# Performance work log

Hardware: AMD Instinct MI355X
Metric: run time of the kernel (lower is better)

Reference implementation:

```python
import jax, jax.numpy as jnp
import numpy as np

MARGIN = 0.5


def setup_inputs() -> dict:
    key = jax.random.key(0)
    k1, k2, k3, k4 = jax.random.split(key, 4)
    Ns, Nt, D = 8192, 8192, 512
    return {
        "source_emb": jax.random.normal(k1, (Ns, D), dtype=jnp.float32),
        "target_emb": jax.random.normal(k2, (Nt, D), dtype=jnp.float32),
        "source_sec": jax.random.randint(k3, (Ns,), 0, 6),
        "target_sec": jax.random.randint(k4, (Nt,), 0, 6),
    }


def reference(source_emb, target_emb, source_sec, target_sec):
    D = source_emb.shape[-1]
    Nt = target_emb.shape[0]
    sq_s = jnp.sum(source_emb * source_emb, axis=-1)  # [Ns]
    sq_t = jnp.sum(target_emb * target_emb, axis=-1)  # [Nt]
    gram = jnp.einsum("sd,td->st", source_emb, target_emb)  # [Ns, Nt]
    d2 = jnp.maximum(sq_s[:, None] + sq_t[None, :] - 2.0 * gram, 0.0) / D
    d = jnp.sqrt(d2)
    same = source_sec[:, None] == target_sec[None, :]  # [Ns, Nt] bool
    # semantic: sum of d^2 over matching pairs, divided by Nt
    loss_s = jnp.sum(jnp.where(same, d2, 0.0), axis=1) / Nt
    # contrastive: sum of max(0, margin - d)^2 over non-matching pairs, / Nt
    hinge = jnp.maximum(0.0, MARGIN - d) ** 2
    loss_c = jnp.sum(jnp.where(same, 0.0, hinge), axis=1) / Nt
    return (loss_s, loss_c)
```

## Files before the change

### kernel.cpp

```cpp
#include <hip/hip_runtime.h>
#include <stdint.h>
#include <stddef.h>

#define NS 8192
#define NT 8192
#define DD 512
#define QS 32.0f
#define INV_S2 (1.0f / (QS * QS))
#define INV_DNT (1.0f / ((float)DD * (float)NT))
#define INV_NT  (1.0f / (float)NT)

typedef __attribute__((ext_vector_type(4))) int i32x4;
typedef __attribute__((ext_vector_type(16))) int i32x16;

#define WS_A    ((size_t)0)
#define WS_B    (WS_A + (size_t)NS * DD)
#define WS_SQS  (WS_B + (size_t)NT * DD)
#define WS_SQT  (WS_SQS + (size_t)NS * 4)

__device__ __forceinline__ void gload16(const void* g, void* l) {
  __builtin_amdgcn_global_load_lds(
      (const __attribute__((address_space(1))) unsigned int*)g,
      (__attribute__((address_space(3))) unsigned int*)l, 16, 0, 0);
}

__global__ __launch_bounds__(256) void prep_kernel(
    const float* __restrict__ src, const float* __restrict__ tgt,
    char* __restrict__ ws) {
  const int tid = threadIdx.x, wid = tid >> 6, lane = tid & 63;
  char* Ai8 = ws + WS_A;
  char* Bi8 = ws + WS_B;
  float* sqs = (float*)(ws + WS_SQS);
  float* sqt = (float*)(ws + WS_SQT);

#pragma unroll
  for (int it = 0; it < 4; ++it) {
    const int row = blockIdx.x * 4 + wid + it * 4096;
    const bool isT = row >= NS;
    const int r = isT ? row - NS : row;
    const float* in = (isT ? tgt : src) + (size_t)r * DD;
    const float4* rp = (const float4*)in;
    float4 v0 = rp[lane * 2], v1 = rp[lane * 2 + 1];
    float x[8] = {v0.x, v0.y, v0.z, v0.w, v1.x, v1.y, v1.z, v1.w};
    float ss = 0.f;
    int q[8];
#pragma unroll
    for (int j = 0; j < 8; ++j) {
      ss += x[j] * x[j];
      int qi = __float2int_rn(x[j] * QS);
      q[j] = min(127, max(-127, qi));
    }
    const int lo = (q[0] & 255) | ((q[1] & 255) << 8) |
                   ((q[2] & 255) << 16) | ((q[3] & 255) << 24);
    const int hi = (q[4] & 255) | ((q[5] & 255) << 8) |
                   ((q[6] & 255) << 16) | ((q[7] & 255) << 24);
    *(int2*)((isT ? Bi8 : Ai8) + (size_t)r * DD + lane * 8) = make_int2(lo, hi);
#pragma unroll
    for (int off = 32; off >= 1; off >>= 1) ss += __shfl_xor(ss, off, 64);
    if (lane == 0) (isT ? sqt : sqs)[r] = ss;
  }
}

__global__ __launch_bounds__(256, 2) void gram_kernel(
    const char* __restrict__ ws, const int* __restrict__ ssec,
    const int* __restrict__ tsec, float* __restrict__ out) {
  __shared__ __align__(16) char As[8192];
  __shared__ __align__(16) char Bs[8192];
  __shared__ float ls_red[2][128];
  __shared__ float sq_l[128];
  __shared__ int sec_l[128];

  const float* sqs = (const float*)(ws + WS_SQS);
  const float* sqt = (const float*)(ws + WS_SQT);

  const int lin = blockIdx.x;
  const int xcd = lin & 7, ii = lin >> 3;
  const int m_blk = xcd * 8 + (ii & 7);
  const int n_blk = ii >> 3;
  const int rowA = m_blk * 128, rowB = n_blk * 128;

  const int tid = threadIdx.x, wid = tid >> 6, lane = tid & 63;
  const int wr = wid >> 1, wc = wid & 1;
  const int lh = lane >> 5;

  const char* aSrc[2];
  const char* bSrc[2];
  int ldsDst[2];
#pragma unroll
  for (int ih = 0; ih < 2; ++ih) {
    const int o = ih * 4096 + tid * 16;
    const int row_p = o >> 6;
    const int bl = (o & 63) ^ (((row_p >> 1) & 3) << 4);
    ldsDst[ih] = ih * 4096 + wid * 1024;
    aSrc[ih] = ws + WS_A + (size_t)(rowA + row_p) * DD + bl;
    bSrc[ih] = ws + WS_B + (size_t)(rowB + row_p) * DD + bl;
  }

  int aOff[2][2], bOff[2][2];
#pragma unroll
  for (int mi = 0; mi < 2; ++mi)
#pragma unroll
    for (int kk = 0; kk < 2; ++kk) {
      const int l = kk * 32 + lh * 16;
      const int ra = wr * 64 + mi * 32 + (lane & 31);
      aOff[mi][kk] = ra * 64 + (l ^ (((ra >> 1) & 3) << 4));
      const int rb = wc * 64 + mi * 32 + (lane & 31);
      bOff[mi][kk] = rb * 64 + (l ^ (((rb >> 1) & 3) << 4));
    }

  i32x16 acc[2][2];
#pragma unroll
  for (int mi = 0; mi < 2; ++mi)
#pragma unroll
    for (int ni = 0; ni < 2; ++ni)
#pragma unroll
      for (int j = 0; j < 16; ++j) acc[mi][ni][j] = 0;

  for (int t = 0; t < 8; ++t) {
    const size_t k0 = (size_t)t * 64;
    gload16(aSrc[0] + k0, &As[ldsDst[0]]);
    gload16(aSrc[1] + k0, &As[ldsDst[1]]);
    gload16(bSrc[0] + k0, &Bs[ldsDst[0]]);
    gload16(bSrc[1] + k0, &Bs[ldsDst[1]]);
    __syncthreads();

    i32x4 a[2][2], b[2][2];
#pragma unroll
    for (int mi = 0; mi < 2; ++mi)
#pragma unroll
      for (int kk = 0; kk < 2; ++kk) {
        a[mi][kk] = *(const i32x4*)&As[aOff[mi][kk]];
        b[mi][kk] = *(const i32x4*)&Bs[bOff[mi][kk]];
      }
#pragma unroll
    for (int kk = 0; kk < 2; ++kk)
#pragma unroll
      for (int mi = 0; mi < 2; ++mi)
#pragma unroll
        for (int ni = 0; ni < 2; ++ni)
          acc[mi][ni] = __builtin_amdgcn_mfma_i32_32x32x32_i8(
              a[mi][kk], b[ni][kk], acc[mi][ni], 0, 0, 0);
    __syncthreads();
  }

  if (tid < 128) {
    sq_l[tid] = sqs[rowA + tid];
    sec_l[tid] = ssec[rowA + tid];
  }
  __syncthreads();

  float sqc[2];
  int tc[2];
#pragma unroll
  for (int ni = 0; ni < 2; ++ni) {
    const int gcol = rowB + wc * 64 + ni * 32 + (lane & 31);
    sqc[ni] = sqt[gcol];
    tc[ni] = tsec[gcol];
  }

#pragma unroll
  for (int mi = 0; mi < 2; ++mi) {
#pragma unroll
    for (int reg = 0; reg < 16; ++reg) {
      const int rowin = (reg & 3) + 8 * (reg >> 2) + 4 * lh;
      const int lrow = wr * 64 + mi * 32 + rowin;
      const float sqr = sq_l[lrow];
      const int sc = sec_l[lrow];
      float v = 0.f;
#pragma unroll
      for (int ni = 0; ni < 2; ++ni) {
        const float g = (float)acc[mi][ni][reg] * INV_S2;
        const float d2r = sqr + sqc[ni] - 2.f * g;
        if (sc == tc[ni]) {
          v += fmaxf(d2r, 0.f);
        } else if (d2r < 128.f) {
          const float d = sqrtf(fmaxf(d2r, 0.f) * (1.f / (float)DD));
          const float hh = 0.5f - d;
          atomicAdd(&out[NS + rowA + lrow], hh * hh * INV_NT);
        }
      }
      v += __shfl_xor(v, 1, 64);
      v += __shfl_xor(v, 2, 64);
      v += __shfl_xor(v, 4, 64);
      v += __shfl_xor(v, 8, 64);
      v += __shfl_xor(v, 16, 64);
      if ((lane & 31) == rowin) ls_red[wc][lrow] = v;
    }
  }
  __syncthreads();

  if (tid < 128)
    atomicAdd(&out[rowA + tid], (ls_red[0][tid] + ls_red[1][tid]) * INV_DNT);
}

extern "C" void kernel_launch(void* const* d_in, const int* in_sizes, int n_in,
                              void* d_out, int out_size, void* d_ws, size_t ws_size,
                              hipStream_t stream) {
  const float* src = (const float*)d_in[0];
  const float* tgt = (const float*)d_in[1];
  const int* ssec = (const int*)d_in[2];
  const int* tsec = (const int*)d_in[3];
  float* out = (float*)d_out;
  char* ws = (char*)d_ws;

  hipMemsetAsync(out, 0, (size_t)2 * NS * sizeof(float), stream);
  prep_kernel<<<1024, 256, 0, stream>>>(src, tgt, ws);
  gram_kernel<<<4096, 256, 0, stream>>>(ws, ssec, tsec, out);
}
```

Baseline: 94.62 us.

## Compute semantic loss via per-section target sums and skip epilogue tiles by bound

The semantic loss is computed algebraically from per-section target sums, counts and squared-norm sums, using a new reduction kernel and a per-row dot-product kernel, rather than in the gram epilogue. The gram kernel gains a three-stage LDS prefetch pipeline with explicit waitcnt and barriers. Its epilogue uses a wave-level bound check that skips tiles whose distances all exceed the margin, keeping only a negative-clamp correction for matching pairs. This removes most of the per-element epilogue work and shuffle reductions, at the cost of two extra launches, more atomics and more LDS per block.

```diff
diff --git a/kernel.cpp b/kernel.cpp
--- a/kernel.cpp
+++ b/kernel.cpp
@@ -5,6 +5,7 @@
 #define NS 8192
 #define NT 8192
 #define DD 512
+#define NSEC 6
 #define QS 32.0f
 #define INV_S2 (1.0f / (QS * QS))
 #define INV_DNT (1.0f / ((float)DD * (float)NT))
@@ -17,6 +18,10 @@
 #define WS_B    (WS_A + (size_t)NS * DD)
 #define WS_SQS  (WS_B + (size_t)NT * DD)
 #define WS_SQT  (WS_SQS + (size_t)NS * 4)
+#define WS_TS   (WS_SQT + (size_t)NT * 4)
+#define WS_CNT  (WS_TS + (size_t)NSEC * DD * 4)
+#define WS_SSQ  (WS_CNT + NSEC * 4)
+#define WS_ZEND (WS_SSQ + NSEC * 4)
 
 __device__ __forceinline__ void gload16(const void* g, void* l) {
   __builtin_amdgcn_global_load_lds(
@@ -61,14 +66,83 @@
   }
 }
 
-__global__ __launch_bounds__(256, 2) void gram_kernel(
+__global__ __launch_bounds__(512) void tsum_kernel(
+    const float* __restrict__ tgt, const int* __restrict__ tsec,
+    char* __restrict__ ws) {
+  const int d = threadIdx.x;
+  const int r0 = blockIdx.x * 128;
+  float a[NSEC] = {0.f, 0.f, 0.f, 0.f, 0.f, 0.f};
+  for (int r = 0; r < 128; ++r) {
+    const int sec = tsec[r0 + r];
+    const float v = tgt[(size_t)(r0 + r) * DD + d];
+#pragma unroll
+    for (int c = 0; c < NSEC; ++c) a[c] += (sec == c) ? v : 0.f;
+  }
+  float* ts = (float*)(ws + WS_TS);
+#pragma unroll
+  for (int c = 0; c < NSEC; ++c) atomicAdd(&ts[c * DD + d], a[c]);
+
+  if (threadIdx.x < 64) {
+    const float* sqt = (const float*)(ws + WS_SQT);
+    float cn[NSEC] = {0, 0, 0, 0, 0, 0}, sq[NSEC] = {0, 0, 0, 0, 0, 0};
+#pragma unroll
+    for (int i = 0; i < 2; ++i) {
+      const int r = r0 + i * 64 + threadIdx.x;
+      const int sec = tsec[r];
+      const float qv = sqt[r];
+#pragma unroll
+      for (int c = 0; c < NSEC; ++c) {
+        cn[c] += (sec == c) ? 1.f : 0.f;
+        sq[c] += (sec == c) ? qv : 0.f;
+      }
+    }
+#pragma unroll
+    for (int c = 0; c < NSEC; ++c) {
+#pragma unroll
+      for (int off = 32; off >= 1; off >>= 1) {
+        cn[c] += __shfl_xor(cn[c], off, 64);
+        sq[c] += __shfl_xor(sq[c], off, 64);
+      }
+    }
+    if (threadIdx.x == 0) {
+      float* cnt = (float*)(ws + WS_CNT);
+      float* ssq = (float*)(ws + WS_SSQ);
+#pragma unroll
+      for (int c = 0; c < NSEC; ++c) {
+        atomicAdd(&cnt[c], cn[c]);
+        atomicAdd(&ssq[c], sq[c]);
+      }
+    }
+  }
+}
+
+__global__ __launch_bounds__(256) void ls_kernel(
+    const float* __restrict__ src, const int* __restrict__ ssec,
+    const char* __restrict__ ws, float* __restrict__ out) {
+  const int tid = threadIdx.x, wid = tid >> 6, lane = tid & 63;
+  const int row = blockIdx.x * 4 + wid;
+  const float* tsum = (const float*)(ws + WS_TS);
+  const float* cnt  = (const float*)(ws + WS_CNT);
+  const float* ssq  = (const float*)(ws + WS_SSQ);
+  const float* sqs  = (const float*)(ws + WS_SQS);
+
+  const int c = ssec[row];
+  const float4* rp = (const float4*)(src + (size_t)row * DD);
+  const float4* tp = (const float4*)(tsum + c * DD);
+  float4 a0 = rp[lane * 2], a1 = rp[lane * 2 + 1];
+  float4 b0 = tp[lane * 2], b1 = tp[lane * 2 + 1];
+  float dot = a0.x * b0.x + a0.y * b0.y + a0.z * b0.z + a0.w * b0.w +
+              a1.x * b1.x + a1.y * b1.y + a1.z * b1.z + a1.w * b1.w;
+#pragma unroll
+  for (int off = 32; off >= 1; off >>= 1) dot += __shfl_xor(dot, off, 64);
+  if (lane == 0)
+    out[row] = (cnt[c] * sqs[row] + ssq[c] - 2.f * dot) * INV_DNT;
+}
+
+__global__ __launch_bounds__(256, 3) void gram_kernel(
     const char* __restrict__ ws, const int* __restrict__ ssec,
     const int* __restrict__ tsec, float* __restrict__ out) {
-  __shared__ __align__(16) char As[8192];
-  __shared__ __align__(16) char Bs[8192];
-  __shared__ float ls_red[2][128];
-  __shared__ float sq_l[128];
-  __shared__ int sec_l[128];
+  __shared__ __align__(16) char lds[3][16384];
 
   const float* sqs = (const float*)(ws + WS_SQS);
   const float* sqt = (const float*)(ws + WS_SQT);
@@ -96,6 +170,14 @@
     bSrc[ih] = ws + WS_B + (size_t)(rowB + row_p) * DD + bl;
   }
 
+#define STAGE(T, BUF)                                                   \
+  {                                                                     \
+    gload16(aSrc[0] + (size_t)(T) * 64, &lds[BUF][ldsDst[0]]);          \
+    gload16(aSrc[1] + (size_t)(T) * 64, &lds[BUF][ldsDst[1]]);          \
+    gload16(bSrc[0] + (size_t)(T) * 64, &lds[BUF][8192 + ldsDst[0]]);   \
+    gload16(bSrc[1] + (size_t)(T) * 64, &lds[BUF][8192 + ldsDst[1]]);   \
+  }
+
   int aOff[2][2], bOff[2][2];
 #pragma unroll
   for (int mi = 0; mi < 2; ++mi)
@@ -105,7 +187,7 @@
       const int ra = wr * 64 + mi * 32 + (lane & 31);
       aOff[mi][kk] = ra * 64 + (l ^ (((ra >> 1) & 3) << 4));
       const int rb = wc * 64 + mi * 32 + (lane & 31);
-      bOff[mi][kk] = rb * 64 + (l ^ (((rb >> 1) & 3) << 4));
+      bOff[mi][kk] = 8192 + rb * 64 + (l ^ (((rb >> 1) & 3) << 4));
     }
 
   i32x16 acc[2][2];
@@ -116,21 +198,24 @@
 #pragma unroll
       for (int j = 0; j < 16; ++j) acc[mi][ni][j] = 0;
 
+  STAGE(0, 0)
+  STAGE(1, 1)
+  asm volatile("s_waitcnt vmcnt(4)" ::: "memory");
+  __builtin_amdgcn_sched_barrier(0);
+  __builtin_amdgcn_s_barrier();
+
+#pragma unroll
   for (int t = 0; t < 8; ++t) {
-    const size_t k0 = (size_t)t * 64;
-    gload16(aSrc[0] + k0, &As[ldsDst[0]]);
-    gload16(aSrc[1] + k0, &As[ldsDst[1]]);
-    gload16(bSrc[0] + k0, &Bs[ldsDst[0]]);
-    gload16(bSrc[1] + k0, &Bs[ldsDst[1]]);
-    __syncthreads();
+    const int cur = t % 3;
+    if (t + 2 < 8) STAGE(t + 2, (t + 2) % 3)
 
     i32x4 a[2][2], b[2][2];
 #pragma unroll
     for (int mi = 0; mi < 2; ++mi)
 #pragma unroll
       for (int kk = 0; kk < 2; ++kk) {
-        a[mi][kk] = *(const i32x4*)&As[aOff[mi][kk]];
-        b[mi][kk] = *(const i32x4*)&Bs[bOff[mi][kk]];
+        a[mi][kk] = *(const i32x4*)&lds[cur][aOff[mi][kk]];
+        b[mi][kk] = *(const i32x4*)&lds[cur][bOff[mi][kk]];
       }
 #pragma unroll
     for (int kk = 0; kk < 2; ++kk)
@@ -140,57 +225,70 @@
         for (int ni = 0; ni < 2; ++ni)
           acc[mi][ni] = __builtin_amdgcn_mfma_i32_32x32x32_i8(
               a[mi][kk], b[ni][kk], acc[mi][ni], 0, 0, 0);
-    __syncthreads();
-  }
-
-  if (tid < 128) {
-    sq_l[tid] = sqs[rowA + tid];
-    sec_l[tid] = ssec[rowA + tid];
-  }
-  __syncthreads();
-
+
+    __builtin_amdgcn_sched_barrier(0);
+    if (t + 2 < 8) {
+      asm volatile("s_waitcnt vmcnt(4)" ::: "memory");
+    } else if (t == 6) {
+      asm volatile("s_waitcnt vmcnt(0)" ::: "memory");
+    }
+    __builtin_amdgcn_sched_barrier(0);
+    if (t < 7) __builtin_amdgcn_s_barrier();
+  }
+#undef STAGE
+
+  const int colc = lane & 31;
   float sqc[2];
-  int tc[2];
-#pragma unroll
-  for (int ni = 0; ni < 2; ++ni) {
-    const int gcol = rowB + wc * 64 + ni * 32 + (lane & 31);
-    sqc[ni] = sqt[gcol];
-    tc[ni] = tsec[gcol];
-  }
-
-#pragma unroll
-  for (int mi = 0; mi < 2; ++mi) {
-#pragma unroll
-    for (int reg = 0; reg < 16; ++reg) {
-      const int rowin = (reg & 3) + 8 * (reg >> 2) + 4 * lh;
-      const int lrow = wr * 64 + mi * 32 + rowin;
-      const float sqr = sq_l[lrow];
-      const int sc = sec_l[lrow];
-      float v = 0.f;
-#pragma unroll
-      for (int ni = 0; ni < 2; ++ni) {
-        const float g = (float)acc[mi][ni][reg] * INV_S2;
-        const float d2r = sqr + sqc[ni] - 2.f * g;
-        if (sc == tc[ni]) {
-          v += fmaxf(d2r, 0.f);
-        } else if (d2r < 128.f) {
-          const float d = sqrtf(fmaxf(d2r, 0.f) * (1.f / (float)DD));
-          const float hh = 0.5f - d;
-          atomicAdd(&out[NS + rowA + lrow], hh * hh * INV_NT);
+#pragma unroll
+  for (int ni = 0; ni < 2; ++ni)
+    sqc[ni] = sqt[rowB + wc * 64 + ni * 32 + colc];
+
+  float smin = sqs[rowA + wr * 64 + lane];
+#pragma unroll
+  for (int off = 32; off >= 1; off >>= 1)
+    smin = fminf(smin, __shfl_xor(smin, off, 64));
+
+  int thr[2];
+#pragma unroll
+  for (int ni = 0; ni < 2; ++ni)
+    thr[ni] = (int)((smin + sqc[ni] - 129.0f) * 512.0f);
+
+  int mx0 = (int)0x80000000, mx1 = (int)0x80000000;
+#pragma unroll
+  for (int mi = 0; mi < 2; ++mi)
+#pragma unroll
+    for (int j = 0; j < 16; ++j) {
+      mx0 = max(mx0, acc[mi][0][j]);
+      mx1 = max(mx1, acc[mi][1][j]);
+    }
+
+  if (__any((mx0 > thr[0]) || (mx1 > thr[1]))) {
+#pragma unroll
+    for (int mi = 0; mi < 2; ++mi) {
+#pragma unroll
+      for (int j = 0; j < 16; ++j) {
+        const int rowin = (j & 3) + 8 * (j >> 2) + 4 * lh;
+        const int grow = rowA + wr * 64 + mi * 32 + rowin;
+        const float sqr = sqs[grow];
+        const int sc = ssec[grow];
+#pragma unroll
+        for (int ni = 0; ni < 2; ++ni) {
+          const int gcol = rowB + wc * 64 + ni * 32 + colc;
+          const float d2r =
+              sqr + sqc[ni] - 2.f * (float)acc[mi][ni][j] * INV_S2;
+          if (d2r < 128.f) {
+            if (sc != tsec[gcol]) {
+              const float d = sqrtf(fmaxf(d2r, 0.f) * (1.f / (float)DD));
+              const float hh = 0.5f - d;
+              atomicAdd(&out[NS + grow], hh * hh * INV_NT);
+            } else if (d2r < 0.f) {
+              atomicAdd(&out[grow], -d2r * INV_DNT);
+            }
+          }
         }
       }
-      v += __shfl_xor(v, 1, 64);
-      v += __shfl_xor(v, 2, 64);
-      v += __shfl_xor(v, 4, 64);
-      v += __shfl_xor(v, 8, 64);
-      v += __shfl_xor(v, 16, 64);
-      if ((lane & 31) == rowin) ls_red[wc][lrow] = v;
-    }
-  }
-  __syncthreads();
-
-  if (tid < 128)
-    atomicAdd(&out[rowA + tid], (ls_red[0][tid] + ls_red[1][tid]) * INV_DNT);
+    }
+  }
 }
 
 extern "C" void kernel_launch(void* const* d_in, const int* in_sizes, int n_in,
@@ -203,7 +301,10 @@
   float* out = (float*)d_out;
   char* ws = (char*)d_ws;
 
-  hipMemsetAsync(out, 0, (size_t)2 * NS * sizeof(float), stream);
+  hipMemsetAsync(ws + WS_TS, 0, (size_t)(WS_ZEND - WS_TS), stream);
+  hipMemsetAsync(out + NS, 0, (size_t)NS * sizeof(float), stream);
   prep_kernel<<<1024, 256, 0, stream>>>(src, tgt, ws);
+  tsum_kernel<<<64, 512, 0, stream>>>(tgt, tsec, ws);
+  ls_kernel<<<2048, 256, 0, stream>>>(src, ssec, ws, out);
   gram_kernel<<<4096, 256, 0, stream>>>(ws, ssec, tsec, out);
 }
```

After: 86.74 us. 8.3% less time.
